# Kernel tuning notes

Measured on AMD Instinct MI355X. Metric: run time of the kernel, lower is better.

Reference implementation:

```python
import jax, jax.numpy as jnp
import numpy as np

SIZE, D, N, E = 50000, 1024, 50000, 100000


def setup_inputs() -> dict:
    key = jax.random.key(0)
    k1, k2 = jax.random.split(key)
    # torchhd.embeddings.Random produces bipolar {-1,+1} MAP hypervectors
    w = jnp.where(jax.random.uniform(k1, (SIZE, D)) < 0.5, -1.0, 1.0).astype(jnp.float32)
    edge_index = jax.random.randint(k2, (2, E), 0, N, dtype=jnp.int32)
    return {"node_ids_weight": w, "edge_index": edge_index, "num_nodes": N}


def reference(node_ids_weight, edge_index, num_nodes):
    # degree_centrality: in-degree via bincount on columns, normalized
    col = edge_index[1]
    degree = jnp.bincount(col, length=num_nodes)
    pr = degree / num_nodes  # float
    pr_argsort = jnp.argsort(pr)  # stable sort, matches torch sort semantics on ties

    # node_id_hvs[pr_argsort] = weight[:num_nodes]  (scatter assign)
    node_id_hvs = jnp.zeros((num_nodes, node_ids_weight.shape[1]),
                            dtype=node_ids_weight.dtype)
    node_id_hvs = node_id_hvs.at[pr_argsort].set(node_ids_weight[:num_nodes])

    # to_undirected: sort endpoints per edge, then unique columns.
    # jit-friendly unique: lexsort edges, mask out duplicates of the previous edge.
    e = jnp.sort(edge_index, axis=0)  # [2, E], row <= col per edge
    order = jnp.lexsort((e[1], e[0]))
    r = e[0][order]
    c = e[1][order]
    keep = jnp.concatenate([
        jnp.array([True]),
        (r[1:] != r[:-1]) | (c[1:] != c[:-1]),
    ])  # [E] True for first occurrence of each unique edge

    # bind = elementwise multiply of gathered hvs; multiset = sum over edges
    hvs = node_id_hvs[r] * node_id_hvs[c]  # [E, D]
    out = jnp.sum(jnp.where(keep[:, None], hvs, 0.0), axis=0)  # [D]
    return out
```

## Files before the change

kernel.cpp:

```cpp
#include <hip/hip_runtime.h>
#include <stdint.h>

#define DCAP   128
#define CHUNK  256
#define LOG_TAB 19
#define TAB_SIZE (1u << LOG_TAB)
#define TAB_MASK (TAB_SIZE - 1u)
#define KEMPTY 0xFFFFFFFFu

__global__ __launch_bounds__(256) void k_init(uint4* __restrict__ z, int zn4,
                                              uint4* __restrict__ t, int tn4) {
    int stride = gridDim.x * 256;
    int i = blockIdx.x * 256 + threadIdx.x;
    uint4 zero = make_uint4(0u, 0u, 0u, 0u);
    uint4 ones = make_uint4(~0u, ~0u, ~0u, ~0u);
    for (int j = i; j < zn4; j += stride) z[j] = zero;
    for (int j = i; j < tn4; j += stride) t[j] = ones;
}

__global__ void k_degree(const int* __restrict__ col, int* __restrict__ degree, int E) {
    int e = blockIdx.x * blockDim.x + threadIdx.x;
    if (e < E) atomicAdd(&degree[col[e]], 1);
}

__global__ void k_chunk_hist(const int* __restrict__ degree, int* __restrict__ hist,
                             int* __restrict__ chunkHist, int N) {
    __shared__ int sh[DCAP];
    int t = threadIdx.x;
    if (t < DCAP) sh[t] = 0;
    __syncthreads();
    int j = blockIdx.x * CHUNK + t;
    if (j < N) {
        int d = degree[j];
        if (d < DCAP) atomicAdd(&sh[d], 1);
        else          atomicAdd(&hist[d], 1);
    }
    __syncthreads();
    if (t < DCAP) chunkHist[blockIdx.x * DCAP + t] = sh[t];
}

__global__ void k_chunk_prefix(int* __restrict__ hist, int* __restrict__ chunkHist,
                               int numChunks) {
    __shared__ int stot[DCAP];
    int d = threadIdx.x;
    int tot = 0;
    for (int c = 0; c < numChunks; ++c) tot += chunkHist[c * DCAP + d];
    stot[d] = tot;
    hist[d] = tot;
    __syncthreads();
    int run = 0;
    for (int d2 = 0; d2 < d; ++d2) run += stot[d2];
    for (int c = 0; c < numChunks; ++c) {
        int tmp = chunkHist[c * DCAP + d];
        chunkHist[c * DCAP + d] = run;
        run += tmp;
    }
}

__global__ void k_pos_small(const int* __restrict__ degree, const int* __restrict__ chunkBase,
                            int* __restrict__ pos, int N) {
    __shared__ int sdeg[CHUNK];
    int t = threadIdx.x;
    int j = blockIdx.x * CHUNK + t;
    int d = (j < N) ? degree[j] : -1;
    sdeg[t] = d;
    __syncthreads();
    if (j < N && d < DCAP) {
        int r = 0;
        for (int t2 = 0; t2 < t; ++t2) r += (sdeg[t2] == d);
        pos[j] = chunkBase[blockIdx.x * DCAP + d] + r;
    }
}

__global__ void k_pos_large(const int* __restrict__ degree, const int* __restrict__ hist,
                            int* __restrict__ pos, int N, int E) {
    int d = DCAP + blockIdx.x * blockDim.x + threadIdx.x;
    if (d > E) return;
    if (hist[d] == 0) return;
    int base = 0;
    for (int d2 = 0; d2 < d; ++d2) base += hist[d2];
    int cnt = 0;
    for (int j = 0; j < N; ++j)
        if (degree[j] == d) pos[j] = base + cnt++;
}

__global__ __launch_bounds__(256) void k_pack_ballot(const float* __restrict__ W,
                                                     uint32_t* __restrict__ Wbits,
                                                     long long G) {
    long long wv0 = ((long long)blockIdx.x * 256 + threadIdx.x) >> 6;
    long long nwv = ((long long)gridDim.x * 256) >> 6;
    int lane = threadIdx.x & 63;
    int k = lane >> 1, half = lane & 1;
    const uint4* W4 = (const uint4*)W;
    for (long long gb = wv0 * 4; gb < G; gb += nwv * 4) {
        #pragma unroll
        for (int s = 0; s < 4; ++s) {
            long long g = gb + s;
            if (g < G) {
                uint4 u = W4[g * 64 + lane];
                unsigned long long m0 = __ballot((int)u.x < 0);
                unsigned long long m1 = __ballot((int)u.y < 0);
                unsigned long long m2 = __ballot((int)u.z < 0);
                unsigned long long m3 = __ballot((int)u.w < 0);
                if (lane < 8) {
                    unsigned long long m = (k == 0) ? m0 : (k == 1) ? m1
                                         : (k == 2) ? m2 : m3;
                    Wbits[g * 8 + lane] = half ? (uint32_t)(m >> 32) : (uint32_t)m;
                }
            }
        }
    }
}

__global__ __launch_bounds__(256) void k_pack_linear(const float* __restrict__ W,
                                                     uint32_t* __restrict__ Wbits, long long NW) {
    long long widx = (long long)blockIdx.x * 256 + threadIdx.x;
    if (widx >= NW) return;
    const uint4* src = (const uint4*)(W + widx * 32);
    uint32_t word = 0;
    #pragma unroll
    for (int q = 0; q < 8; ++q) {
        uint4 u = src[q];
        word |= (u.x >> 31) << (4 * q + 0);
        word |= (u.y >> 31) << (4 * q + 1);
        word |= (u.z >> 31) << (4 * q + 2);
        word |= (u.w >> 31) << (4 * q + 3);
    }
    Wbits[widx] = word;
}

__global__ void k_insert(const int* __restrict__ ei, const int* __restrict__ pos,
                         unsigned int* __restrict__ tab, int* __restrict__ uA,
                         int* __restrict__ uB, int* __restrict__ count, int E) {
    int e = blockIdx.x * blockDim.x + threadIdx.x;
    if (e >= E) return;
    int a = ei[e], b = ei[E + e];
    int r = min(a, b), c = max(a, b);
    unsigned int key = ((unsigned int)r << 16) | (unsigned int)c;
    unsigned int h = (key * 2654435761u) >> (32 - LOG_TAB);
    while (true) {
        unsigned int old = atomicCAS(&tab[h], KEMPTY, key);
        if (old == KEMPTY) {
            int idx = atomicAdd(count, 1);
            uA[idx] = pos[r];
            uB[idx] = pos[c];
            return;
        }
        if (old == key) return;
        h = (h + 1) & TAB_MASK;
    }
}

__global__ __launch_bounds__(256) void k_accum_bits(const uint32_t* __restrict__ Wbits,
                                                    const int* __restrict__ uA,
                                                    const int* __restrict__ uB,
                                                    const int* __restrict__ count,
                                                    int* __restrict__ neg, int D) {
    __shared__ int sneg[1024];
    int t = threadIdx.x;
    int w = t & 31;
    int slot = t >> 5;
    int wpr = D / 32;
    for (int i = t; i < D; i += 256) sneg[i] = 0;
    __syncthreads();
    int cnt = *count;
    int cnts[32];
    #pragma unroll
    for (int d = 0; d < 32; ++d) cnts[d] = 0;
    for (int base = blockIdx.x * 8; base < cnt; base += gridDim.x * 8) {
        int e = base + slot;
        if (e < cnt) {
            uint32_t a = Wbits[(size_t)uA[e] * wpr + w];
            uint32_t b = Wbits[(size_t)uB[e] * wpr + w];
            uint32_t x = a ^ b;
            #pragma unroll
            for (int d = 0; d < 32; ++d) cnts[d] += (x >> d) & 1u;
        }
    }
    #pragma unroll
    for (int d = 0; d < 32; ++d) atomicAdd(&sneg[w * 32 + d], cnts[d]);
    __syncthreads();
    for (int i = t; i < D; i += 256)
        if (sneg[i]) atomicAdd(&neg[i], sneg[i]);
}

__global__ void k_finalize(const int* __restrict__ neg, const int* __restrict__ count,
                           float* __restrict__ out, int D, int permuted) {
    int d = blockIdx.x * blockDim.x + threadIdx.x;
    if (d >= D) return;
    int ni;
    if (permuted) {
        int off = d & 255, q = d >> 8;
        int k = off & 3, l = off >> 2, half = l >> 5, b = l & 31;
        ni = (q * 8 + 2 * k + half) * 32 + b;
    } else {
        ni = d;
    }
    out[d] = (float)(*count - 2 * neg[ni]);
}

static inline size_t align256(size_t x) { return (x + 255) & ~(size_t)255; }

extern "C" void kernel_launch(void* const* d_in, const int* in_sizes, int n_in,
                              void* d_out, int out_size, void* d_ws, size_t ws_size,
                              hipStream_t stream) {
    const float* W  = (const float*)d_in[0];
    const int*   ei = (const int*)d_in[1];
    const int D = out_size;
    const int N = in_sizes[0] / D;
    const int E = in_sizes[1] / 2;
    const int numChunks = (N + CHUNK - 1) / CHUNK;
    const long long ND = (long long)N * D;
    const long long NW = ND / 32;

    char* p = (char*)d_ws;
    char* zbase = p;
    int* degree       = (int*)p;          p += align256((size_t)N * 4);
    int* hist         = (int*)p;          p += align256((size_t)(E + 1) * 4);
    int* count        = (int*)p;          p += 256;
    int* neg          = (int*)p;          p += align256((size_t)D * 4);
    size_t zbytes = (size_t)(p - zbase);
    int* chunkHist    = (int*)p;          p += align256((size_t)numChunks * DCAP * 4);
    int* pos          = (int*)p;          p += align256((size_t)N * 4);
    unsigned int* tab = (unsigned int*)p; p += (size_t)TAB_SIZE * 4;
    int* uA           = (int*)p;          p += align256((size_t)E * 4);
    int* uB           = (int*)p;          p += align256((size_t)E * 4);
    uint32_t* Wbits   = (uint32_t*)p;     p += align256((size_t)NW * 4);

    int zn4 = (int)(zbytes / 16);
    int tn4 = (int)((size_t)TAB_SIZE * 4 / 16);
    int initGrid = (max(zn4, tn4) + 255) / 256;
    k_init<<<initGrid, 256, 0, stream>>>((uint4*)zbase, zn4, (uint4*)tab, tn4);

    k_degree<<<(E + 255) / 256, 256, 0, stream>>>(ei + E, degree, E);
    k_chunk_hist<<<numChunks, CHUNK, 0, stream>>>(degree, hist, chunkHist, N);
    k_chunk_prefix<<<1, DCAP, 0, stream>>>(hist, chunkHist, numChunks);
    k_pos_small<<<numChunks, CHUNK, 0, stream>>>(degree, chunkHist, pos, N);
    int nLarge = E + 1 - DCAP;
    k_pos_large<<<(nLarge + 255) / 256, 256, 0, stream>>>(degree, hist, pos, N, E);

    int permuted = (D % 256 == 0);
    if (permuted) {
        long long G = ND / 256;
        k_pack_ballot<<<2048, 256, 0, stream>>>(W, Wbits, G);
    } else {
        k_pack_linear<<<(int)((NW + 255) / 256), 256, 0, stream>>>(W, Wbits, NW);
    }

    k_insert<<<(E + 255) / 256, 256, 0, stream>>>(ei, pos, tab, uA, uB, count, E);
    k_accum_bits<<<1024, 256, 0, stream>>>(Wbits, uA, uB, count, neg, D);
    k_finalize<<<(D + 255) / 256, 256, 0, stream>>>(neg, count, (float*)d_out, D, permuted);
}
```

Before: 160.3 us.

## Deepen ballot-pack loads, merge position kernels, and use memsets for init

The bit-packing kernel now issues eight independent 16-byte loads per wave before ballotting, to raise memory-level parallelism over the large weight matrix. The two position kernels merge into one launch, and the custom init kernel gives way to two hipMemsetAsync calls. The chunk size grows from 256 to 1024, which cuts the number of chunks but lengthens the quadratic per-thread rank loop in shared memory. It also raises register pressure in the pack kernel.

```diff
diff --git a/kernel.cpp b/kernel.cpp
--- a/kernel.cpp
+++ b/kernel.cpp
@@ -2,21 +2,11 @@
 #include <stdint.h>
 
 #define DCAP   128
-#define CHUNK  256
+#define CHUNK  1024
 #define LOG_TAB 19
 #define TAB_SIZE (1u << LOG_TAB)
 #define TAB_MASK (TAB_SIZE - 1u)
 #define KEMPTY 0xFFFFFFFFu
-
-__global__ __launch_bounds__(256) void k_init(uint4* __restrict__ z, int zn4,
-                                              uint4* __restrict__ t, int tn4) {
-    int stride = gridDim.x * 256;
-    int i = blockIdx.x * 256 + threadIdx.x;
-    uint4 zero = make_uint4(0u, 0u, 0u, 0u);
-    uint4 ones = make_uint4(~0u, ~0u, ~0u, ~0u);
-    for (int j = i; j < zn4; j += stride) z[j] = zero;
-    for (int j = i; j < tn4; j += stride) t[j] = ones;
-}
 
 __global__ void k_degree(const int* __restrict__ col, int* __restrict__ degree, int E) {
     int e = blockIdx.x * blockDim.x + threadIdx.x;
@@ -57,33 +47,36 @@
     }
 }
 
-__global__ void k_pos_small(const int* __restrict__ degree, const int* __restrict__ chunkBase,
-                            int* __restrict__ pos, int N) {
-    __shared__ int sdeg[CHUNK];
+__global__ __launch_bounds__(CHUNK) void k_pos(const int* __restrict__ degree,
+                                               const int* __restrict__ chunkBase,
+                                               const int* __restrict__ hist,
+                                               int* __restrict__ pos,
+                                               int N, int E, int numChunks) {
     int t = threadIdx.x;
-    int j = blockIdx.x * CHUNK + t;
-    int d = (j < N) ? degree[j] : -1;
-    sdeg[t] = d;
-    __syncthreads();
-    if (j < N && d < DCAP) {
-        int r = 0;
-        for (int t2 = 0; t2 < t; ++t2) r += (sdeg[t2] == d);
-        pos[j] = chunkBase[blockIdx.x * DCAP + d] + r;
-    }
-}
-
-__global__ void k_pos_large(const int* __restrict__ degree, const int* __restrict__ hist,
-                            int* __restrict__ pos, int N, int E) {
-    int d = DCAP + blockIdx.x * blockDim.x + threadIdx.x;
-    if (d > E) return;
-    if (hist[d] == 0) return;
-    int base = 0;
-    for (int d2 = 0; d2 < d; ++d2) base += hist[d2];
-    int cnt = 0;
-    for (int j = 0; j < N; ++j)
-        if (degree[j] == d) pos[j] = base + cnt++;
-}
-
+    if ((int)blockIdx.x < numChunks) {
+        __shared__ int sdeg[CHUNK];
+        int j = blockIdx.x * CHUNK + t;
+        int d = (j < N) ? degree[j] : -1;
+        sdeg[t] = d;
+        __syncthreads();
+        if (j < N && d < DCAP && d >= 0) {
+            int r = 0;
+            for (int t2 = 0; t2 < t; ++t2) r += (sdeg[t2] == d);
+            pos[j] = chunkBase[blockIdx.x * DCAP + d] + r;
+        }
+    } else {
+        int d = DCAP + (blockIdx.x - numChunks) * CHUNK + t;
+        if (d > E) return;
+        if (hist[d] == 0) return;
+        int base = 0;
+        for (int d2 = 0; d2 < d; ++d2) base += hist[d2];
+        int cnt = 0;
+        for (int j = 0; j < N; ++j)
+            if (degree[j] == d) pos[j] = base + cnt++;
+    }
+}
+
+#define PACK_DEPTH 8
 __global__ __launch_bounds__(256) void k_pack_ballot(const float* __restrict__ W,
                                                      uint32_t* __restrict__ Wbits,
                                                      long long G) {
@@ -92,21 +85,25 @@
     int lane = threadIdx.x & 63;
     int k = lane >> 1, half = lane & 1;
     const uint4* W4 = (const uint4*)W;
-    for (long long gb = wv0 * 4; gb < G; gb += nwv * 4) {
+    for (long long gb = wv0 * PACK_DEPTH; gb < G; gb += nwv * PACK_DEPTH) {
+        uint4 u[PACK_DEPTH];
         #pragma unroll
-        for (int s = 0; s < 4; ++s) {
+        for (int s = 0; s < PACK_DEPTH; ++s) {
             long long g = gb + s;
-            if (g < G) {
-                uint4 u = W4[g * 64 + lane];
-                unsigned long long m0 = __ballot((int)u.x < 0);
-                unsigned long long m1 = __ballot((int)u.y < 0);
-                unsigned long long m2 = __ballot((int)u.z < 0);
-                unsigned long long m3 = __ballot((int)u.w < 0);
-                if (lane < 8) {
-                    unsigned long long m = (k == 0) ? m0 : (k == 1) ? m1
-                                         : (k == 2) ? m2 : m3;
-                    Wbits[g * 8 + lane] = half ? (uint32_t)(m >> 32) : (uint32_t)m;
-                }
+            if (g >= G) g = G - 1;
+            u[s] = W4[g * 64 + lane];
+        }
+        #pragma unroll
+        for (int s = 0; s < PACK_DEPTH; ++s) {
+            long long g = gb + s;
+            unsigned long long m0 = __ballot((int)u[s].x < 0);
+            unsigned long long m1 = __ballot((int)u[s].y < 0);
+            unsigned long long m2 = __ballot((int)u[s].z < 0);
+            unsigned long long m3 = __ballot((int)u[s].w < 0);
+            if (g < G && lane < 8) {
+                unsigned long long m = (k == 0) ? m0 : (k == 1) ? m1
+                                     : (k == 2) ? m2 : m3;
+                Wbits[g * 8 + lane] = half ? (uint32_t)(m >> 32) : (uint32_t)m;
             }
         }
     }
@@ -227,17 +224,15 @@
     int* uB           = (int*)p;          p += align256((size_t)E * 4);
     uint32_t* Wbits   = (uint32_t*)p;     p += align256((size_t)NW * 4);
 
-    int zn4 = (int)(zbytes / 16);
-    int tn4 = (int)((size_t)TAB_SIZE * 4 / 16);
-    int initGrid = (max(zn4, tn4) + 255) / 256;
-    k_init<<<initGrid, 256, 0, stream>>>((uint4*)zbase, zn4, (uint4*)tab, tn4);
+    hipMemsetAsync(zbase, 0, zbytes, stream);
+    hipMemsetAsync(tab, 0xFF, (size_t)TAB_SIZE * 4, stream);
 
     k_degree<<<(E + 255) / 256, 256, 0, stream>>>(ei + E, degree, E);
     k_chunk_hist<<<numChunks, CHUNK, 0, stream>>>(degree, hist, chunkHist, N);
     k_chunk_prefix<<<1, DCAP, 0, stream>>>(hist, chunkHist, numChunks);
-    k_pos_small<<<numChunks, CHUNK, 0, stream>>>(degree, chunkHist, pos, N);
-    int nLarge = E + 1 - DCAP;
-    k_pos_large<<<(nLarge + 255) / 256, 256, 0, stream>>>(degree, hist, pos, N, E);
+    int nLargeBlocks = (E + 1 - DCAP + CHUNK - 1) / CHUNK;
+    k_pos<<<numChunks + nLargeBlocks, CHUNK, 0, stream>>>(degree, chunkHist, hist,
+                                                          pos, N, E, numChunks);
 
     int permuted = (D % 256 == 0);
     if (permuted) {
```

Result: faster. 137.2 us (-14.4%).
